# Kernel tuning notes

Measured on AMD Instinct MI355X. Metric: run time of the kernel, lower is better.

## Reference

```python
import jax, jax.numpy as jnp
import numpy as np

B, C, T = 4, 256, 2048
H, G = 4, 8          # num_heads, groupnorm groups
HD = C // H          # head_dim = 64
EPS = 1e-5


def setup_inputs() -> dict:
    key = jax.random.key(0)
    ks = jax.random.split(key, 7)
    return {
        "x": jax.random.normal(ks[0], (B, C, T), dtype=jnp.float32),
        "gn_w": jnp.ones((C,), jnp.float32) + 0.02 * jax.random.normal(ks[1], (C,), jnp.float32),
        "gn_b": 0.02 * jax.random.normal(ks[2], (C,), jnp.float32),
        "w_qkv": 0.02 * jax.random.normal(ks[3], (3 * C, C), jnp.float32),
        "b_qkv": 0.02 * jax.random.normal(ks[4], (3 * C,), jnp.float32),
        "w_out": 0.02 * jax.random.normal(ks[5], (C, C), jnp.float32),
        "b_out": 0.02 * jax.random.normal(ks[6], (C,), jnp.float32),
    }


def reference(x, gn_w, gn_b, w_qkv, b_qkv, w_out, b_out):
    b, c, t = x.shape
    scale = HD ** -0.5
    # GroupNorm over (channels-in-group, T) per (batch, group)
    xg = x.reshape(b, G, c // G, t)
    mu = jnp.mean(xg, axis=(2, 3), keepdims=True)
    var = jnp.var(xg, axis=(2, 3), keepdims=True)
    h = ((xg - mu) * jax.lax.rsqrt(var + EPS)).reshape(b, c, t)
    h = h * gn_w[None, :, None] + gn_b[None, :, None]
    h = h.transpose(0, 2, 1)                       # [B, T, C]
    qkv = h @ w_qkv.T + b_qkv                      # [B, T, 3C]
    q, k, v = jnp.split(qkv, 3, axis=-1)
    to_heads = lambda z: z.reshape(b, t, H, HD).transpose(0, 2, 1, 3)  # [B, H, T, HD]
    q, k, v = map(to_heads, (q, k, v))
    sim = jnp.einsum('bhid,bhjd->bhij', q, k) * scale   # [B, H, T, T]
    attn = jax.nn.softmax(sim, axis=-1)
    out = jnp.einsum('bhij,bhjd->bhid', attn, v)        # [B, H, T, HD]
    out = out.transpose(0, 2, 1, 3).reshape(b, t, c)    # [B, T, C]
    out = out @ w_out.T + b_out
    return x + out.transpose(0, 2, 1)                   # [B, C, T]
```

## Files before the change

### kernel.cpp

```cpp
#include <hip/hip_runtime.h>

#define NTHREADS 256

typedef __attribute__((ext_vector_type(8))) short bf16x8;
typedef __attribute__((ext_vector_type(4))) float f32x4;

constexpr int Bx = 4, Cx = 256, Tx = 2048, Hx = 4, Gx = 8, HDx = 64, CGx = 32;
constexpr float EPSx = 1e-5f;
constexpr float QSCALE = 0.125f * 1.44269504088896340736f;
constexpr float SHIFT = 16.0f;

__device__ __forceinline__ float bf2f(short s) {
  union { unsigned u; float f; } c;
  c.u = ((unsigned)(unsigned short)s) << 16;
  return c.f;
}
__device__ __forceinline__ short f2bf(float f) {
  union { float f; unsigned u; } c; c.f = f;
  unsigned r = c.u + 0x7fffu + ((c.u >> 16) & 1u);
  return (short)(r >> 16);
}
__device__ __forceinline__ unsigned cvtpk(float lo, float hi) {
  unsigned r;
  asm("v_cvt_pk_bf16_f32 %0, %1, %2" : "=v"(r) : "v"(lo), "v"(hi));
  return r;
}
__device__ __forceinline__ float fexp2(float x) { return __builtin_amdgcn_exp2f(x); }
__device__ __forceinline__ void gload16(const void* g, void* l) {
  __builtin_amdgcn_global_load_lds((const __attribute__((address_space(1))) void*)g,
                                   (__attribute__((address_space(3))) void*)l, 16, 0, 0);
}

__global__ void k_pre(const float* __restrict__ x, float2* __restrict__ part,
                      const float* __restrict__ wq, const float* __restrict__ wo,
                      short* __restrict__ oq, short* __restrict__ oo) {
  if (blockIdx.x < Bx * Gx * 8) {
    int blk = blockIdx.x;
    const f32x4* xv = (const f32x4*)(x + (size_t)blk * 8192);
    float s = 0.f, ss = 0.f;
    for (int i = threadIdx.x; i < 2048; i += NTHREADS) {
      f32x4 v = xv[i];
      s += v[0] + v[1] + v[2] + v[3];
      ss += v[0]*v[0] + v[1]*v[1] + v[2]*v[2] + v[3]*v[3];
    }
    #pragma unroll
    for (int m = 32; m >= 1; m >>= 1) { s += __shfl_xor(s, m, 64); ss += __shfl_xor(ss, m, 64); }
    __shared__ float ls[4], lss[4];
    int wid = threadIdx.x >> 6;
    if ((threadIdx.x & 63) == 0) { ls[wid] = s; lss[wid] = ss; }
    __syncthreads();
    if (threadIdx.x == 0) {
      float S = 0.f, SS = 0.f;
      #pragma unroll
      for (int w = 0; w < 4; w++) { S += ls[w]; SS += lss[w]; }
      part[blk] = make_float2(S, SS);
    }
  } else {
    int i = (blockIdx.x - Bx * Gx * 8) * NTHREADS + threadIdx.x;
    if (i < 3 * Cx * Cx) oq[i] = f2bf(wq[i]);
    else oo[i - 3 * Cx * Cx] = f2bf(wo[i - 3 * Cx * Cx]);
  }
}

__global__ void k_gn_apply(const float* __restrict__ x, const float* __restrict__ gw,
                           const float* __restrict__ gb, const float2* __restrict__ part,
                           short* __restrict__ h) {
  int b = blockIdx.z, c0 = blockIdx.y * 32, t0 = blockIdx.x * 32;
  int g = c0 >> 5;
  float S = 0.f, SS = 0.f;
  #pragma unroll
  for (int j = 0; j < 8; j++) { float2 p = part[(b * Gx + g) * 8 + j]; S += p.x; SS += p.y; }
  float inv = 1.f / (float)(CGx * Tx);
  float mu = S * inv;
  float rs = rsqrtf(SS * inv - mu * mu + EPSx);

  __shared__ float tile[32][33];
  int tx = threadIdx.x & 31, ty = threadIdx.x >> 5;
  #pragma unroll
  for (int i = 0; i < 4; i++) {
    int cl = ty + i * 8;
    int c = c0 + cl;
    float v = x[((size_t)b * Cx + c) * Tx + t0 + tx];
    tile[cl][tx] = (v - mu) * rs * gw[c] + gb[c];
  }
  __syncthreads();
  #pragma unroll
  for (int i = 0; i < 4; i++) {
    int tl = ty + i * 8;
    h[((size_t)b * Tx + t0 + tl) * Cx + c0 + tx] = f2bf(tile[tx][tl]);
  }
}

__global__ __launch_bounds__(256) void k_gemm_qkv(
    const short* __restrict__ A, const short* __restrict__ Bt,
    const float* __restrict__ bias, short* __restrict__ qg,
    short* __restrict__ kgo, short* __restrict__ vtg) {
  constexpr int K = 256;
  __shared__ short tlt[64][66];
  int wid = threadIdx.x >> 6, lane = threadIdx.x & 63;
  int m0 = blockIdx.x * 64 + wid * 16;
  int n0 = blockIdx.y * 64;
  int row = lane & 15, kg = lane >> 4;
  f32x4 acc[4] = {};
  const short* Ap = A + (size_t)(m0 + row) * K + kg * 8;
  const short* Bp0 = Bt + (size_t)(n0 + row) * K + kg * 8;
  #pragma unroll
  for (int k = 0; k < K; k += 32) {
    bf16x8 af = *(const bf16x8*)(Ap + k);
    #pragma unroll
    for (int nt = 0; nt < 4; nt++) {
      bf16x8 bf = *(const bf16x8*)(Bp0 + (size_t)nt * 16 * K + k);
      acc[nt] = __builtin_amdgcn_mfma_f32_16x16x32_bf16(af, bf, acc[nt], 0, 0, 0);
    }
  }
  int sec = n0 >> 8, hh = (n0 >> 6) & 3;
  int bB = (blockIdx.x * 64) >> 11, t0 = (blockIdx.x * 64) & (Tx - 1);
  if (sec < 2) {
    #pragma unroll
    for (int nt = 0; nt < 4; nt++)
      #pragma unroll
      for (int r = 0; r < 4; r++) {
        int m = m0 + kg * 4 + r;
        int n = n0 + nt * 16 + row;
        int b = m >> 11, t = m & (Tx - 1), hd = n & 63;
        float v = acc[nt][r] + bias[n];
        if (sec == 0)
          qg[(((size_t)b * Hx + hh) * Tx + t) * 64 + hd] = f2bf(v * QSCALE);
        else
          kgo[(((size_t)b * Hx + hh) * Tx + t) * 64 + hd] = f2bf(v);
      }
  } else {
    int tl = wid * 16 + kg * 4;
    #pragma unroll
    for (int nt = 0; nt < 4; nt++) {
      int n = n0 + nt * 16 + row;
      float bn = bias[n];
      int hd = nt * 16 + row;
      *(unsigned*)&tlt[hd][tl]     = cvtpk(acc[nt][0] + bn, acc[nt][1] + bn);
      *(unsigned*)&tlt[hd][tl + 2] = cvtpk(acc[nt][2] + bn, acc[nt][3] + bn);
    }
    __syncthreads();
    int hd = threadIdx.x >> 2, tch = (threadIdx.x & 3) * 16;
    short* vr = vtg + (((size_t)bB * Hx + hh) * 64 + hd) * Tx + t0 + tch;
    #pragma unroll
    for (int j = 0; j < 16; j += 2) *(unsigned*)(vr + j) = *(unsigned*)&tlt[hd][tch + j];
  }
}

#define KVB 64
__global__ __launch_bounds__(256) void k_attn(const short* __restrict__ qg,
                                              const short* __restrict__ kgl,
                                              const short* __restrict__ vtg,
                                              short* __restrict__ po,
                                              float* __restrict__ ps,
                                              int zshift) {
  __shared__ short lds[16384];
  const int bid = blockIdx.x;
  const int nsplit = 1 << zshift;
  const int g = bid & ((16 << zshift) - 1);
  const int sp = g & (nsplit - 1);
  const int bh = g >> zshift;
  const int kvlen = Tx >> zshift;
  const int kvbase = sp * kvlen;
  const int wid = threadIdx.x >> 6, lane = threadIdx.x & 63;
  const int row = lane & 15, kg4 = lane >> 4;
  const int q0 = (bid >> (4 + zshift)) * 128 + wid * 32;
  const short* qbase = qg + (size_t)bh * Tx * 64;
  const short* kbase = kgl + (size_t)bh * Tx * 64;
  const short* vbase = vtg + (size_t)bh * 64 * Tx;

  bf16x8 qf[2][2];
  #pragma unroll
  for (int qs = 0; qs < 2; ++qs)
    #pragma unroll
    for (int c = 0; c < 2; ++c)
      qf[qs][c] = *(const bf16x8*)(qbase + (size_t)(q0 + qs * 16 + row) * 64 + c * 32 + kg4 * 8);

  const int idx0 = wid * 64 + lane, idx1 = idx0 + 256;
  const int rr0 = idx0 >> 3, sl0 = (idx0 & 7) ^ (rr0 & 7);
  const int rr1 = idx1 >> 3, sl1 = (idx1 & 7) ^ (rr1 & 7);
  const short* ks0 = kbase + (size_t)(kvbase + rr0) * 64 + sl0 * 8;
  const short* ks1 = kbase + (size_t)(kvbase + rr1) * 64 + sl1 * 8;
  const short* vs0 = vbase + (size_t)rr0 * Tx + kvbase + sl0 * 8;
  const short* vs1 = vbase + (size_t)rr1 * Tx + kvbase + sl1 * 8;
  short* const kd0 = lds + wid * 512;
  short* const kd1 = lds + wid * 512 + 2048;
  short* const vd0 = lds + 8192 + wid * 512;
  short* const vd1 = lds + 8192 + wid * 512 + 2048;
  auto stage = [&](int sbuf, int itn) {
    const int ko = itn * 4096, vo = itn * 64, so = sbuf * 4096;
    gload16(ks0 + ko, kd0 + so);
    gload16(ks1 + ko, kd1 + so);
    gload16(vs0 + vo, vd0 + so);
    gload16(vs1 + vo, vd1 + so);
  };

  const int swz = row & 7;
  const int kc0 = (kg4 ^ swz) * 8;
  const int kc1 = ((4 + kg4) ^ swz) * 8;
  const int sA0 = ((0 + (kg4 >> 1)) ^ swz) * 8 + (kg4 & 1) * 4;
  const int sA1 = ((2 + (kg4 >> 1)) ^ swz) * 8 + (kg4 & 1) * 4;
  const int sB0 = ((4 + (kg4 >> 1)) ^ swz) * 8 + (kg4 & 1) * 4;
  const int sB1 = ((6 + (kg4 >> 1)) ^ swz) * 8 + (kg4 & 1) * 4;
  int vro[4], kro[4];
  #pragma unroll
  for (int nt = 0; nt < 4; ++nt) { vro[nt] = (nt * 16 + row) * 64; kro[nt] = vro[nt]; }

  float l0 = 0.f, l1 = 0.f;
  f32x4 oa0[4] = {}, oa1[4] = {};
  const int nit = kvlen / KVB;

  stage(0, 0);
  for (int it = 0; it < nit; ++it) {
    const int cur = it & 1;
    if (it + 1 < nit) {
      stage(cur ^ 1, it + 1);
      asm volatile("s_waitcnt vmcnt(4)" ::: "memory");
    } else {
      asm volatile("s_waitcnt vmcnt(0)" ::: "memory");
    }
    __builtin_amdgcn_s_barrier();

    const short* Kb = lds + (cur << 12);
    const short* Vb = lds + 8192 + (cur << 12);

    f32x4 a0[4], a1[4];
    __builtin_amdgcn_s_setprio(1);
    #pragma unroll
    for (int t = 0; t < 4; ++t) {
      const short* kr = Kb + kro[t];
      bf16x8 kf0 = *(const bf16x8*)(kr + kc0);
      bf16x8 kf1 = *(const bf16x8*)(kr + kc1);
      f32x4 x0 = {-SHIFT, -SHIFT, -SHIFT, -SHIFT};
      f32x4 x1 = {-SHIFT, -SHIFT, -SHIFT, -SHIFT};
      x0 = __builtin_amdgcn_mfma_f32_16x16x32_bf16(kf0, qf[0][0], x0, 0, 0, 0);
      x0 = __builtin_amdgcn_mfma_f32_16x16x32_bf16(kf1, qf[0][1], x0, 0, 0, 0);
      x1 = __builtin_amdgcn_mfma_f32_16x16x32_bf16(kf0, qf[1][0], x1, 0, 0, 0);
      x1 = __builtin_amdgcn_mfma_f32_16x16x32_bf16(kf1, qf[1][1], x1, 0, 0, 0);
      a0[t] = x0; a1[t] = x1;
    }
    __builtin_amdgcn_s_setprio(0);

    union U { unsigned u[4]; bf16x8 v; };
    U a00, a01, a10, a11;
    float rs0 = 0.f, rs1 = 0.f;
    #pragma unroll
    for (int t = 0; t < 4; ++t) {
      float e0 = fexp2(a0[t][0]), e1 = fexp2(a0[t][1]);
      float e2 = fexp2(a0[t][2]), e3 = fexp2(a0[t][3]);
      rs0 += (e0 + e1) + (e2 + e3);
      unsigned w0 = cvtpk(e0, e1), w1 = cvtpk(e2, e3);
      if (t < 2) { a00.u[t * 2] = w0; a00.u[t * 2 + 1] = w1; }
      else       { a01.u[(t - 2) * 2] = w0; a01.u[(t - 2) * 2 + 1] = w1; }
      float f0 = fexp2(a1[t][0]), f1 = fexp2(a1[t][1]);
      float f2 = fexp2(a1[t][2]), f3 = fexp2(a1[t][3]);
      rs1 += (f0 + f1) + (f2 + f3);
      unsigned y0 = cvtpk(f0, f1), y1 = cvtpk(f2, f3);
      if (t < 2) { a10.u[t * 2] = y0; a10.u[t * 2 + 1] = y1; }
      else       { a11.u[(t - 2) * 2] = y0; a11.u[(t - 2) * 2 + 1] = y1; }
    }
    l0 += rs0; l1 += rs1;

    __builtin_amdgcn_s_setprio(1);
    #pragma unroll
    for (int nt = 0; nt < 4; ++nt) {
      const short* vr = Vb + vro[nt];
      union { unsigned long long q[2]; bf16x8 v; } vf0, vf1;
      vf0.q[0] = *(const unsigned long long*)(vr + sA0);
      vf0.q[1] = *(const unsigned long long*)(vr + sA1);
      vf1.q[0] = *(const unsigned long long*)(vr + sB0);
      vf1.q[1] = *(const unsigned long long*)(vr + sB1);
      oa0[nt] = __builtin_amdgcn_mfma_f32_16x16x32_bf16(a00.v, vf0.v, oa0[nt], 0, 0, 0);
      oa1[nt] = __builtin_amdgcn_mfma_f32_16x16x32_bf16(a10.v, vf0.v, oa1[nt], 0, 0, 0);
      oa0[nt] = __builtin_amdgcn_mfma_f32_16x16x32_bf16(a01.v, vf1.v, oa0[nt], 0, 0, 0);
      oa1[nt] = __builtin_amdgcn_mfma_f32_16x16x32_bf16(a11.v, vf1.v, oa1[nt], 0, 0, 0);
    }
    __builtin_amdgcn_s_setprio(0);
    __builtin_amdgcn_s_barrier();
  }

  l0 += __shfl_xor(l0, 16, 64); l0 += __shfl_xor(l0, 32, 64);
  l1 += __shfl_xor(l1, 16, 64); l1 += __shfl_xor(l1, 32, 64);
  float li0[4], li1[4];
  #pragma unroll
  for (int r = 0; r < 4; ++r) {
    li0[r] = 1.f / __shfl(l0, kg4 * 4 + r, 64);
    li1[r] = 1.f / __shfl(l1, kg4 * 4 + r, 64);
  }
  short* pob = po + (((size_t)sp * 16 + bh) * Tx) * 64;
  #pragma unroll
  for (int nt = 0; nt < 4; ++nt)
    #pragma unroll
    for (int r = 0; r < 4; ++r) {
      int t = q0 + kg4 * 4 + r;
      pob[(size_t)t * 64 + nt * 16 + row] = f2bf(oa0[nt][r] * li0[r]);
      pob[(size_t)(t + 16) * 64 + nt * 16 + row] = f2bf(oa1[nt][r] * li1[r]);
    }
  if (kg4 == 0) {
    float* psb = ps + ((size_t)sp * 16 + bh) * Tx;
    psb[q0 + row] = SHIFT + __log2f(l0);
    psb[q0 + 16 + row] = SHIFT + __log2f(l1);
  }
}

__global__ __launch_bounds__(256) void k_merge(const short* __restrict__ po,
                                               const float* __restrict__ ps,
                                               short* __restrict__ aout, int nsplit) {
  int gid = blockIdx.x * 256 + threadIdx.x;
  int dc = gid & 7;
  int q = (gid >> 3) & (Tx - 1);
  int bh = gid >> 14;
  float s[4];
  float maxs = -1e30f;
  for (int i = 0; i < nsplit; ++i) {
    s[i] = ps[((size_t)i * 16 + bh) * Tx + q];
    maxs = fmaxf(maxs, s[i]);
  }
  float acc[8] = {};
  float denom = 0.f;
  for (int i = 0; i < nsplit; ++i) {
    float w = fexp2(s[i] - maxs);
    denom += w;
    bf16x8 v = *(const bf16x8*)(po + (((size_t)i * 16 + bh) * Tx + q) * 64 + dc * 8);
    #pragma unroll
    for (int j = 0; j < 8; ++j) acc[j] += w * bf2f(v[j]);
  }
  float dinv = 1.f / denom;
  union { unsigned u[4]; bf16x8 v; } o;
  #pragma unroll
  for (int j = 0; j < 4; ++j) o.u[j] = cvtpk(acc[2 * j] * dinv, acc[2 * j + 1] * dinv);
  int b = bh >> 2, h = bh & 3;
  *(bf16x8*)(aout + ((size_t)b * Tx + q) * Cx + h * 64 + dc * 8) = o.v;
}

__global__ __launch_bounds__(256) void k_gemm_proj(
    const short* __restrict__ A, const short* __restrict__ Bt,
    const float* __restrict__ bias, const float* __restrict__ x,
    float* __restrict__ out) {
  constexpr int K = Cx;
  __shared__ float tlt[64][65];
  int wid = threadIdx.x >> 6, lane = threadIdx.x & 63;
  int m0 = blockIdx.x * 64 + wid * 16;
  int n0 = blockIdx.y * 64;
  int row = lane & 15, kg = lane >> 4;
  f32x4 acc[4] = {};
  const short* Ap = A + (size_t)(m0 + row) * K + kg * 8;
  const short* Bp0 = Bt + (size_t)(n0 + row) * K + kg * 8;
  #pragma unroll
  for (int k = 0; k < K; k += 32) {
    bf16x8 af = *(const bf16x8*)(Ap + k);
    #pragma unroll
    for (int nt = 0; nt < 4; nt++) {
      bf16x8 bf = *(const bf16x8*)(Bp0 + (size_t)nt * 16 * K + k);
      acc[nt] = __builtin_amdgcn_mfma_f32_16x16x32_bf16(af, bf, acc[nt], 0, 0, 0);
    }
  }
  #pragma unroll
  for (int nt = 0; nt < 4; nt++) {
    float bn = bias[n0 + nt * 16 + row];
    #pragma unroll
    for (int r = 0; r < 4; r++)
      tlt[nt * 16 + row][wid * 16 + kg * 4 + r] = acc[nt][r] + bn;
  }
  __syncthreads();
  int cl = threadIdx.x >> 2, tch = (threadIdx.x & 3) * 16;
  int mb = blockIdx.x * 64;
  int b = mb >> 11, t0 = mb & (Tx - 1);
  int c = n0 + cl;
  const float* xr = x + ((size_t)b * Cx + c) * Tx + t0 + tch;
  float* orow = out + ((size_t)b * Cx + c) * Tx + t0 + tch;
  #pragma unroll
  for (int j = 0; j < 16; j += 4) {
    f32x4 xv = *(const f32x4*)(xr + j);
    f32x4 v;
    #pragma unroll
    for (int jj = 0; jj < 4; ++jj) v[jj] = xv[jj] + tlt[cl][tch + j + jj];
    *(f32x4*)(orow + j) = v;
  }
}

extern "C" void kernel_launch(void* const* d_in, const int* in_sizes, int n_in,
                              void* d_out, int out_size, void* d_ws, size_t ws_size,
                              hipStream_t stream) {
  const float* x     = (const float*)d_in[0];
  const float* gn_w  = (const float*)d_in[1];
  const float* gn_b  = (const float*)d_in[2];
  const float* w_qkv = (const float*)d_in[3];
  const float* b_qkv = (const float*)d_in[4];
  const float* w_out = (const float*)d_in[5];
  const float* b_out = (const float*)d_in[6];
  float* out = (float*)d_out;

  char* ws = (char*)d_ws;
  size_t off = 0;
  auto alloc = [&](size_t bytes) -> void* {
    void* p = ws + off;
    off += bytes;
    off = (off + 255) & ~(size_t)255;
    return p;
  };
  float2* part  = (float2*)alloc((size_t)Bx * Gx * 8 * sizeof(float2));
  short* h      = (short*)alloc((size_t)Bx * Tx * Cx * 2);
  short* wqkvb  = (short*)alloc((size_t)3 * Cx * Cx * 2);
  short* woutb  = (short*)alloc((size_t)Cx * Cx * 2);
  short* qg     = (short*)alloc((size_t)Bx * Hx * Tx * 64 * 2);
  short* kgo    = (short*)alloc((size_t)Bx * Hx * Tx * 64 * 2);
  short* vtg    = (short*)alloc((size_t)Bx * Hx * 64 * Tx * 2);
  short* aout   = (short*)alloc((size_t)Bx * Tx * Cx * 2);

  size_t per_split = (size_t)16 * Tx * 64 * 2 + (size_t)16 * Tx * sizeof(float) + 512;
  int nsplit = 4, zshift = 2;
  while (nsplit > 1 && off + (size_t)nsplit * per_split > ws_size) { nsplit >>= 1; zshift--; }
  short* po = (short*)alloc((size_t)nsplit * 16 * Tx * 64 * 2);
  float* ps = (float*)alloc((size_t)nsplit * 16 * Tx * sizeof(float));

  k_pre<<<Bx * Gx * 8 + (4 * Cx * Cx + NTHREADS - 1) / NTHREADS, NTHREADS, 0, stream>>>(
      x, part, w_qkv, w_out, wqkvb, woutb);
  k_gn_apply<<<dim3(Tx / 32, Cx / 32, Bx), NTHREADS, 0, stream>>>(x, gn_w, gn_b, part, h);
  k_gemm_qkv<<<dim3(Bx * Tx / 64, 3 * Cx / 64), NTHREADS, 0, stream>>>(h, wqkvb, b_qkv, qg, kgo, vtg);
  k_attn<<<16 * 16 * nsplit, 256, 0, stream>>>(qg, kgo, vtg, po, ps, zshift);
  k_merge<<<(Bx * Hx * Tx * 8) / 256, 256, 0, stream>>>(po, ps, aout, nsplit);
  k_gemm_proj<<<dim3(Bx * Tx / 64, Cx / 64), NTHREADS, 0, stream>>>(aout, woutb, b_out, x, out);
}
```

Before: 89.07 us.

## Fuse split-KV merge into output projection and specialize attention split count

Removes the separate merge kernel and the aout buffer. The projection kernel now reads the per-split partial outputs and scores, does the log-sum-exp weighting in registers, and feeds the result straight into the MFMA projection, using 128-wide output tiles. The attention kernel makes the split count a compile-time constant, unrolls its main loop by two and interleaves exp2 with the QK MFMAs. The trade-offs: the projection grid shrinks to 256 blocks, each block rereads the partials once per 128-column half, and the workspace-size fallback that lowered the split count is gone.

```diff
diff --git a/kernel.cpp b/kernel.cpp
--- a/kernel.cpp
+++ b/kernel.cpp
@@ -7,6 +7,7 @@
 
 constexpr int Bx = 4, Cx = 256, Tx = 2048, Hx = 4, Gx = 8, HDx = 64, CGx = 32;
 constexpr float EPSx = 1e-5f;
+constexpr int NSPLIT = 4, ZSHIFT = 2;
 constexpr float QSCALE = 0.125f * 1.44269504088896340736f;
 constexpr float SHIFT = 16.0f;
 
@@ -152,19 +153,17 @@
                                               const short* __restrict__ kgl,
                                               const short* __restrict__ vtg,
                                               short* __restrict__ po,
-                                              float* __restrict__ ps,
-                                              int zshift) {
+                                              float* __restrict__ ps) {
   __shared__ short lds[16384];
   const int bid = blockIdx.x;
-  const int nsplit = 1 << zshift;
-  const int g = bid & ((16 << zshift) - 1);
-  const int sp = g & (nsplit - 1);
-  const int bh = g >> zshift;
-  const int kvlen = Tx >> zshift;
+  const int g = bid & (16 * NSPLIT - 1);
+  const int sp = g & (NSPLIT - 1);
+  const int bh = g >> ZSHIFT;
+  constexpr int kvlen = Tx / NSPLIT;
   const int kvbase = sp * kvlen;
   const int wid = threadIdx.x >> 6, lane = threadIdx.x & 63;
   const int row = lane & 15, kg4 = lane >> 4;
-  const int q0 = (bid >> (4 + zshift)) * 128 + wid * 32;
+  const int q0 = (bid >> (4 + ZSHIFT)) * 128 + wid * 32;
   const short* qbase = qg + (size_t)bh * Tx * 64;
   const short* kbase = kgl + (size_t)bh * Tx * 64;
   const short* vbase = vtg + (size_t)bh * 64 * Tx;
@@ -202,15 +201,16 @@
   const int sA1 = ((2 + (kg4 >> 1)) ^ swz) * 8 + (kg4 & 1) * 4;
   const int sB0 = ((4 + (kg4 >> 1)) ^ swz) * 8 + (kg4 & 1) * 4;
   const int sB1 = ((6 + (kg4 >> 1)) ^ swz) * 8 + (kg4 & 1) * 4;
-  int vro[4], kro[4];
-  #pragma unroll
-  for (int nt = 0; nt < 4; ++nt) { vro[nt] = (nt * 16 + row) * 64; kro[nt] = vro[nt]; }
+  int vro[4];
+  #pragma unroll
+  for (int nt = 0; nt < 4; ++nt) vro[nt] = (nt * 16 + row) * 64;
 
   float l0 = 0.f, l1 = 0.f;
   f32x4 oa0[4] = {}, oa1[4] = {};
-  const int nit = kvlen / KVB;
+  constexpr int nit = kvlen / KVB;
 
   stage(0, 0);
+  #pragma unroll 2
   for (int it = 0; it < nit; ++it) {
     const int cur = it & 1;
     if (it + 1 < nit) {
@@ -224,11 +224,13 @@
     const short* Kb = lds + (cur << 12);
     const short* Vb = lds + 8192 + (cur << 12);
 
-    f32x4 a0[4], a1[4];
+    union U { unsigned u[4]; bf16x8 v; };
+    U a00, a01, a10, a11;
+    float rs0 = 0.f, rs1 = 0.f;
     __builtin_amdgcn_s_setprio(1);
     #pragma unroll
     for (int t = 0; t < 4; ++t) {
-      const short* kr = Kb + kro[t];
+      const short* kr = Kb + vro[t];
       bf16x8 kf0 = *(const bf16x8*)(kr + kc0);
       bf16x8 kf1 = *(const bf16x8*)(kr + kc1);
       f32x4 x0 = {-SHIFT, -SHIFT, -SHIFT, -SHIFT};
@@ -237,28 +239,21 @@
       x0 = __builtin_amdgcn_mfma_f32_16x16x32_bf16(kf1, qf[0][1], x0, 0, 0, 0);
       x1 = __builtin_amdgcn_mfma_f32_16x16x32_bf16(kf0, qf[1][0], x1, 0, 0, 0);
       x1 = __builtin_amdgcn_mfma_f32_16x16x32_bf16(kf1, qf[1][1], x1, 0, 0, 0);
-      a0[t] = x0; a1[t] = x1;
-    }
-    __builtin_amdgcn_s_setprio(0);
-
-    union U { unsigned u[4]; bf16x8 v; };
-    U a00, a01, a10, a11;
-    float rs0 = 0.f, rs1 = 0.f;
-    #pragma unroll
-    for (int t = 0; t < 4; ++t) {
-      float e0 = fexp2(a0[t][0]), e1 = fexp2(a0[t][1]);
-      float e2 = fexp2(a0[t][2]), e3 = fexp2(a0[t][3]);
+      float e0 = fexp2(x0[0]), e1 = fexp2(x0[1]), e2 = fexp2(x0[2]), e3 = fexp2(x0[3]);
       rs0 += (e0 + e1) + (e2 + e3);
       unsigned w0 = cvtpk(e0, e1), w1 = cvtpk(e2, e3);
-      if (t < 2) { a00.u[t * 2] = w0; a00.u[t * 2 + 1] = w1; }
-      else       { a01.u[(t - 2) * 2] = w0; a01.u[(t - 2) * 2 + 1] = w1; }
-      float f0 = fexp2(a1[t][0]), f1 = fexp2(a1[t][1]);
-      float f2 = fexp2(a1[t][2]), f3 = fexp2(a1[t][3]);
+      float f0 = fexp2(x1[0]), f1 = fexp2(x1[1]), f2 = fexp2(x1[2]), f3 = fexp2(x1[3]);
       rs1 += (f0 + f1) + (f2 + f3);
       unsigned y0 = cvtpk(f0, f1), y1 = cvtpk(f2, f3);
-      if (t < 2) { a10.u[t * 2] = y0; a10.u[t * 2 + 1] = y1; }
-      else       { a11.u[(t - 2) * 2] = y0; a11.u[(t - 2) * 2 + 1] = y1; }
-    }
+      if (t < 2) {
+        a00.u[t * 2] = w0; a00.u[t * 2 + 1] = w1;
+        a10.u[t * 2] = y0; a10.u[t * 2 + 1] = y1;
+      } else {
+        a01.u[(t - 2) * 2] = w0; a01.u[(t - 2) * 2 + 1] = w1;
+        a11.u[(t - 2) * 2] = y0; a11.u[(t - 2) * 2 + 1] = y1;
+      }
+    }
+    __builtin_amdgcn_s_setprio(0);
     l0 += rs0; l1 += rs1;
 
     __builtin_amdgcn_s_setprio(1);
@@ -303,74 +298,81 @@
   }
 }
 
-__global__ __launch_bounds__(256) void k_merge(const short* __restrict__ po,
-                                               const float* __restrict__ ps,
-                                               short* __restrict__ aout, int nsplit) {
-  int gid = blockIdx.x * 256 + threadIdx.x;
-  int dc = gid & 7;
-  int q = (gid >> 3) & (Tx - 1);
-  int bh = gid >> 14;
-  float s[4];
-  float maxs = -1e30f;
-  for (int i = 0; i < nsplit; ++i) {
-    s[i] = ps[((size_t)i * 16 + bh) * Tx + q];
-    maxs = fmaxf(maxs, s[i]);
-  }
-  float acc[8] = {};
-  float denom = 0.f;
-  for (int i = 0; i < nsplit; ++i) {
-    float w = fexp2(s[i] - maxs);
-    denom += w;
-    bf16x8 v = *(const bf16x8*)(po + (((size_t)i * 16 + bh) * Tx + q) * 64 + dc * 8);
-    #pragma unroll
-    for (int j = 0; j < 8; ++j) acc[j] += w * bf2f(v[j]);
-  }
-  float dinv = 1.f / denom;
-  union { unsigned u[4]; bf16x8 v; } o;
-  #pragma unroll
-  for (int j = 0; j < 4; ++j) o.u[j] = cvtpk(acc[2 * j] * dinv, acc[2 * j + 1] * dinv);
-  int b = bh >> 2, h = bh & 3;
-  *(bf16x8*)(aout + ((size_t)b * Tx + q) * Cx + h * 64 + dc * 8) = o.v;
-}
-
-__global__ __launch_bounds__(256) void k_gemm_proj(
-    const short* __restrict__ A, const short* __restrict__ Bt,
-    const float* __restrict__ bias, const float* __restrict__ x,
-    float* __restrict__ out) {
-  constexpr int K = Cx;
-  __shared__ float tlt[64][65];
-  int wid = threadIdx.x >> 6, lane = threadIdx.x & 63;
-  int m0 = blockIdx.x * 64 + wid * 16;
-  int n0 = blockIdx.y * 64;
-  int row = lane & 15, kg = lane >> 4;
-  f32x4 acc[4] = {};
-  const short* Ap = A + (size_t)(m0 + row) * K + kg * 8;
-  const short* Bp0 = Bt + (size_t)(n0 + row) * K + kg * 8;
-  #pragma unroll
-  for (int k = 0; k < K; k += 32) {
-    bf16x8 af = *(const bf16x8*)(Ap + k);
-    #pragma unroll
-    for (int nt = 0; nt < 4; nt++) {
-      bf16x8 bf = *(const bf16x8*)(Bp0 + (size_t)nt * 16 * K + k);
-      acc[nt] = __builtin_amdgcn_mfma_f32_16x16x32_bf16(af, bf, acc[nt], 0, 0, 0);
-    }
-  }
-  #pragma unroll
-  for (int nt = 0; nt < 4; nt++) {
+__global__ __launch_bounds__(256) void k_proj(
+    const short* __restrict__ po, const float* __restrict__ ps,
+    const short* __restrict__ Bt, const float* __restrict__ bias,
+    const float* __restrict__ x, float* __restrict__ out) {
+  __shared__ float tlt[128][65];
+  const int wid = threadIdx.x >> 6, lane = threadIdx.x & 63;
+  const int row = lane & 15, kg = lane >> 4;
+  const int mb = blockIdx.x * 64;
+  const int b = mb >> 11, t0 = mb & (Tx - 1);
+  const int n0 = blockIdx.y * 128;
+  const int t = t0 + wid * 16 + row;
+
+  float wgt[4][NSPLIT], dinv[4];
+  #pragma unroll
+  for (int h = 0; h < 4; ++h) {
+    float s0[NSPLIT], mx = -1e30f;
+    #pragma unroll
+    for (int sp = 0; sp < NSPLIT; ++sp) {
+      s0[sp] = ps[((size_t)sp * 16 + b * 4 + h) * Tx + t];
+      mx = fmaxf(mx, s0[sp]);
+    }
+    float d = 0.f;
+    #pragma unroll
+    for (int sp = 0; sp < NSPLIT; ++sp) { wgt[h][sp] = fexp2(s0[sp] - mx); d += wgt[h][sp]; }
+    dinv[h] = 1.f / d;
+  }
+
+  float a[8][8] = {};
+  #pragma unroll
+  for (int sp = 0; sp < NSPLIT; ++sp) {
+    #pragma unroll
+    for (int j = 0; j < 8; ++j) {
+      int c = j * 32 + kg * 8;
+      int h = c >> 6, d0 = c & 63;
+      const short* q = po + (((size_t)sp * 16 + b * 4 + h) * Tx + t) * 64 + d0;
+      bf16x8 v = *(const bf16x8*)q;
+      float wv = wgt[h][sp];
+      #pragma unroll
+      for (int e = 0; e < 8; ++e) a[j][e] += wv * bf2f(v[e]);
+    }
+  }
+  bf16x8 af[8];
+  #pragma unroll
+  for (int j = 0; j < 8; ++j) {
+    float dv = dinv[(j * 32 + kg * 8) >> 6];
+    union { unsigned u[4]; bf16x8 v; } p;
+    #pragma unroll
+    for (int e = 0; e < 4; ++e) p.u[e] = cvtpk(a[j][2 * e] * dv, a[j][2 * e + 1] * dv);
+    af[j] = p.v;
+  }
+
+  f32x4 acc[8] = {};
+  #pragma unroll
+  for (int j = 0; j < 8; ++j) {
+    #pragma unroll
+    for (int nt = 0; nt < 8; ++nt) {
+      bf16x8 bf = *(const bf16x8*)(Bt + (size_t)(n0 + nt * 16 + row) * 256 + j * 32 + kg * 8);
+      acc[nt] = __builtin_amdgcn_mfma_f32_16x16x32_bf16(af[j], bf, acc[nt], 0, 0, 0);
+    }
+  }
+
+  #pragma unroll
+  for (int nt = 0; nt < 8; ++nt) {
     float bn = bias[n0 + nt * 16 + row];
     #pragma unroll
-    for (int r = 0; r < 4; r++)
+    for (int r = 0; r < 4; ++r)
       tlt[nt * 16 + row][wid * 16 + kg * 4 + r] = acc[nt][r] + bn;
   }
   __syncthreads();
-  int cl = threadIdx.x >> 2, tch = (threadIdx.x & 3) * 16;
-  int mb = blockIdx.x * 64;
-  int b = mb >> 11, t0 = mb & (Tx - 1);
+  int cl = threadIdx.x >> 1, tch = (threadIdx.x & 1) * 32;
   int c = n0 + cl;
   const float* xr = x + ((size_t)b * Cx + c) * Tx + t0 + tch;
   float* orow = out + ((size_t)b * Cx + c) * Tx + t0 + tch;
   #pragma unroll
-  for (int j = 0; j < 16; j += 4) {
+  for (int j = 0; j < 32; j += 4) {
     f32x4 xv = *(const f32x4*)(xr + j);
     f32x4 v;
     #pragma unroll
@@ -406,19 +408,13 @@
   short* qg     = (short*)alloc((size_t)Bx * Hx * Tx * 64 * 2);
   short* kgo    = (short*)alloc((size_t)Bx * Hx * Tx * 64 * 2);
   short* vtg    = (short*)alloc((size_t)Bx * Hx * 64 * Tx * 2);
-  short* aout   = (short*)alloc((size_t)Bx * Tx * Cx * 2);
-
-  size_t per_split = (size_t)16 * Tx * 64 * 2 + (size_t)16 * Tx * sizeof(float) + 512;
-  int nsplit = 4, zshift = 2;
-  while (nsplit > 1 && off + (size_t)nsplit * per_split > ws_size) { nsplit >>= 1; zshift--; }
-  short* po = (short*)alloc((size_t)nsplit * 16 * Tx * 64 * 2);
-  float* ps = (float*)alloc((size_t)nsplit * 16 * Tx * sizeof(float));
+  short* po     = (short*)alloc((size_t)NSPLIT * 16 * Tx * 64 * 2);
+  float* ps     = (float*)alloc((size_t)NSPLIT * 16 * Tx * sizeof(float));
 
   k_pre<<<Bx * Gx * 8 + (4 * Cx * Cx + NTHREADS - 1) / NTHREADS, NTHREADS, 0, stream>>>(
       x, part, w_qkv, w_out, wqkvb, woutb);
   k_gn_apply<<<dim3(Tx / 32, Cx / 32, Bx), NTHREADS, 0, stream>>>(x, gn_w, gn_b, part, h);
   k_gemm_qkv<<<dim3(Bx * Tx / 64, 3 * Cx / 64), NTHREADS, 0, stream>>>(h, wqkvb, b_qkv, qg, kgo, vtg);
-  k_attn<<<16 * 16 * nsplit, 256, 0, stream>>>(qg, kgo, vtg, po, ps, zshift);
-  k_merge<<<(Bx * Hx * Tx * 8) / 256, 256, 0, stream>>>(po, ps, aout, nsplit);
-  k_gemm_proj<<<dim3(Bx * Tx / 64, Cx / 64), NTHREADS, 0, stream>>>(aout, woutb, b_out, x, out);
-}
+  k_attn<<<16 * 16 * NSPLIT, 256, 0, stream>>>(qg, kgo, vtg, po, ps);
+  k_proj<<<dim3(Bx * Tx / 64, 2), NTHREADS, 0, stream>>>(po, ps, woutb, b_out, x, out);
+}
```

Result: no change. 88.52 us (-0.6%).
